# Kernel tuning notes

Measured on AMD Instinct MI355X. Metric: run time of the kernel, lower is better.

Reference implementation:

```python
import jax, jax.numpy as jnp
import numpy as np

B, T, C, H, N = 4, 2048, 1024, 16, 64
CHUNK = 256           # chunk_len
NBSWA = 2             # n_bswa_chunks
BSWA = CHUNK * NBSWA  # sliding window length
SSTATE = CHUNK        # kvm state slots (chunk_len * n_max_d_chunks)
SINK = 1              # sink_len
PARTIAL = 32          # rope_partial_dim
NEG = -1e30


def _ln(x, w, b, eps=1e-5):
    m = x.mean(-1, keepdims=True)
    v = jnp.mean((x - m) ** 2, -1, keepdims=True)
    return (x - m) * jax.lax.rsqrt(v + eps) * w + b


def _rope_tables():
    freq = (1.0 / 10000.0) ** np.linspace(0.0, 1.0, PARTIAL // 2, dtype=np.float32)
    freq = np.repeat(freq, 2)
    freq = np.concatenate([freq, np.zeros(N - PARTIAL, np.float32)])
    th = np.arange(T, dtype=np.float32)[:, None] * freq[None, :]
    cos = np.cos(th)
    sin = np.sin(th)
    sin[:, 1::2] *= -1.0
    return jnp.asarray(cos), jnp.asarray(sin)


def _rope(x, cos, sin):
    # pairwise flip (x0,x1)->(x1,x0)
    xf = x.reshape(*x.shape[:-1], N // 2, 2)[..., ::-1].reshape(x.shape)
    return cos[None, :, None, :] * x + sin[None, :, None, :] * xf


def _forward(residual, x, v1, x0, dx0,
             Wq, Wk, Wv, Wproj, Wkw,
             x_q, x_k, x_v, lamb,
             ln_q_w, ln_q_b, ln_k_w, ln_k_b, ln_dk_w, ln_dk_b, ln_res_w, ln_res_b,
             front_temp, state_temp):
    q = x @ Wq.T
    k = x @ Wk.T
    v = x @ Wv.T
    v = (1.0 - lamb) * v + lamb * v1  # value residual
    q = q.reshape(B, T, H, N)
    k = k.reshape(B, T, H, N)
    v = v.reshape(B, T, H, N)
    q = _ln(q, ln_q_w, ln_q_b)
    k = _ln(k, ln_k_w, ln_k_b)

    def shift(t):  # token shift (use_dkys=True variant)
        return jnp.concatenate([t[:, 0:1], t[:, :-1]], axis=1)

    q = q + x_q[None, None] * (shift(q) - q)
    k = k + x_k[None, None] * (shift(k) - k)
    v = v + x_v[None, None] * (shift(v) - v)

    cos, sin = _rope_tables()
    q = _rope(q, cos, sin)
    k = _rope(k, cos, sin)

    q = q.transpose(0, 2, 1, 3)  # [B,H,T,N]
    k = k.transpose(0, 2, 1, 3)
    v = v.transpose(0, 2, 1, 3)

    kw = jax.nn.sigmoid(jnp.einsum('btc,hc->bht', x, Wkw))[..., None]  # [B,H,T,1]
    st = state_temp.reshape(1, H, 1, 1)
    ft = front_temp.reshape(1, H, 1, 1)

    d_k = jnp.zeros((B, H, SSTATE, N), x.dtype)
    d_v = jnp.zeros((B, H, SSTATE, N), x.dtype)
    d_cnt = jnp.zeros((B, H, SSTATE, 1), x.dtype)
    scale = 1.0 / np.sqrt(N)
    outs = []
    for e in range(CHUNK, T + 1, CHUNK):  # fixed 8 chunks
        qb = e - CHUNK
        bb = max(0, e - BSWA)
        qc = q[:, :, qb:e]
        c_k = k[:, :, bb:bb + CHUNK]
        c_v = v[:, :, bb:bb + CHUNK]
        bk = k[:, :, bb:e]
        bv = v[:, :, bb:e]

        d_k_norm = _ln(d_k, ln_dk_w, ln_dk_b)
        d_vlen = d_cnt  # running count of accumulated c_v vectors per slot
        v_state = d_v / jnp.clip(jnp.linalg.norm(d_v, axis=-1, keepdims=True), 1e-12) * d_vlen
        k_star = jnp.concatenate([d_k_norm * st, bk * ft], axis=-2)
        v_star = jnp.concatenate([v_state, bv], axis=-2)

        qi = np.arange(qb, e)
        ki = np.arange(bb, e)
        mbias = np.where(ki[None, :] <= qi[:, None], 0.0, NEG).astype(np.float32)
        bias = jnp.asarray(np.concatenate([np.zeros((CHUNK, SSTATE), np.float32), mbias], axis=1))

        sc = jnp.einsum('bhqd,bhkd->bhqk', qc, k_star) * scale + bias
        out = jnp.einsum('bhqk,bhkd->bhqd', jax.nn.softmax(sc, axis=-1), v_star)
        outs.append(out)

        # state update: rope_zeroing on first PARTIAL channels, ln_d_k, nearest-slot scatter
        ck0 = jnp.concatenate([jnp.zeros_like(c_k[..., :PARTIAL]), c_k[..., PARTIAL:]], axis=-1)
        ck0 = _ln(ck0, ln_dk_w, ln_dk_b)
        sim = jnp.einsum('bhcd,bhsd->bhcs', ck0, d_k_norm)
        sim = sim.at[..., 0:SINK].set(NEG)
        kwc = kw[:, :, bb:bb + CHUNK]
        ck0 = ck0 * kwc
        cvw = c_v * kwc
        best = jnp.argmax(sim, axis=-1)                       # [B,H,CHUNK]
        oh = jax.nn.one_hot(best, SSTATE, dtype=x.dtype)      # [B,H,CHUNK,S]
        d_k = d_k + jnp.einsum('bhcs,bhcd->bhsd', oh, ck0)
        d_v = d_v + jnp.einsum('bhcs,bhcd->bhsd', oh, cvw)
        d_cnt = d_cnt + oh.sum(axis=2)[..., None]

    y = jnp.concatenate(outs, axis=2).transpose(0, 2, 1, 3).reshape(B, T, C)
    y = _ln(y, ln_res_w, ln_res_b)
    return residual + y @ Wproj.T


def setup_inputs() -> dict:
    key = jax.random.key(0)
    ks = jax.random.split(key, 12)
    f = lambda k, s, sc=1.0: jax.random.normal(k, s, dtype=jnp.float32) * sc
    return {
        'residual': f(ks[0], (B, T, C)),
        'x': f(ks[1], (B, T, C)),
        'v1': f(ks[2], (B, T, C)),
        'x0': f(ks[3], (B, T, C)),
        'dx0': f(ks[4], (B, T, C)),
        'token_ids': jax.random.randint(ks[5], (B, T), 0, 50257),
        'Wq': f(ks[6], (C, C), 0.02),
        'Wk': f(ks[7], (C, C), 0.02),
        'Wv': f(ks[8], (C, C), 0.02),
        'Wproj': f(ks[9], (C, C), 0.02),
        'Wkw': f(ks[10], (H, C), 0.02),
        'x_q': 0.5 * jnp.ones((H, N), jnp.float32),
        'x_k': 0.5 * jnp.ones((H, N), jnp.float32),
        'x_v': 0.5 * jnp.ones((H, N), jnp.float32),
        'lamb': jnp.float32(0.5),
        'ln_q_w': jnp.ones((N,), jnp.float32), 'ln_q_b': jnp.zeros((N,), jnp.float32),
        'ln_k_w': jnp.ones((N,), jnp.float32), 'ln_k_b': jnp.zeros((N,), jnp.float32),
        'ln_dk_w': jnp.ones((N,), jnp.float32), 'ln_dk_b': jnp.zeros((N,), jnp.float32),
        'ln_res_w': jnp.ones((C,), jnp.float32), 'ln_res_b': jnp.zeros((C,), jnp.float32),
        'front_temp': jnp.ones((H,), jnp.float32),
        'state_temp': jnp.ones((H,), jnp.float32),
    }


def reference(residual, x, v1, x0, dx0, token_ids,
              Wq, Wk, Wv, Wproj, Wkw, x_q, x_k, x_v, lamb,
              ln_q_w, ln_q_b, ln_k_w, ln_k_b, ln_dk_w, ln_dk_b, ln_res_w, ln_res_b,
              front_temp, state_temp):
    del token_ids  # unused in visible forward body
    return _forward(residual, x, v1, x0, dx0,
                    Wq, Wk, Wv, Wproj, Wkw,
                    x_q, x_k, x_v, lamb,
                    ln_q_w, ln_q_b, ln_k_w, ln_k_b, ln_dk_w, ln_dk_b, ln_res_w, ln_res_b,
                    front_temp, state_temp)
```

## Files before the change

### kernel.cpp

```cpp
#include <hip/hip_runtime.h>
#include <math.h>

#define Bq 4
#define Tq 2048
#define Cq 1024
#define Hq 16
#define Nq 64

typedef __attribute__((ext_vector_type(8))) short short8v;
typedef __attribute__((ext_vector_type(4))) float f32x4;

__device__ inline float waveSum(float v) {
#pragma unroll
  for (int o = 32; o; o >>= 1) v += __shfl_xor(v, o);
  return v;
}
__device__ inline unsigned short f2bf(float f) {
  unsigned u = __float_as_uint(f);
  unsigned r = (u + 0x7FFFu + ((u >> 16) & 1u)) >> 16;
  return (unsigned short)r;
}
__device__ inline float bf2f(unsigned short b) {
  return __uint_as_float(((unsigned)b) << 16);
}

__global__ __launch_bounds__(256) void f32_to_bf16_kernel(
    const float* __restrict__ src, unsigned short* __restrict__ dst, int n4)
{
  int i = blockIdx.x * 256 + threadIdx.x;
  if (i >= n4) return;
  float4 v = ((const float4*)src)[i];
  ushort4 o;
  o.x = f2bf(v.x); o.y = f2bf(v.y); o.z = f2bf(v.z); o.w = f2bf(v.w);
  ((ushort4*)dst)[i] = o;
}

__global__ __launch_bounds__(256) void f32_to_bf16_hilo_kernel(
    const float* __restrict__ src, unsigned short* __restrict__ hi,
    unsigned short* __restrict__ lo, int n4)
{
  int i = blockIdx.x * 256 + threadIdx.x;
  if (i >= n4) return;
  float4 v = ((const float4*)src)[i];
  ushort4 h, l;
  h.x = f2bf(v.x); l.x = f2bf(v.x - bf2f(h.x));
  h.y = f2bf(v.y); l.y = f2bf(v.y - bf2f(h.y));
  h.z = f2bf(v.z); l.z = f2bf(v.z - bf2f(h.z));
  h.w = f2bf(v.w); l.w = f2bf(v.w - bf2f(h.w));
  ((ushort4*)hi)[i] = h;
  ((ushort4*)lo)[i] = l;
}

__global__ __launch_bounds__(256) void gemm_bf16(
    const unsigned short* __restrict__ A, const unsigned short* __restrict__ W,
    float* __restrict__ dst, const float* __restrict__ extra,
    const float* __restrict__ lamb_p, int mode)
{
  const int m0 = blockIdx.x * 128, n0 = blockIdx.y * 128;
  const int tid = threadIdx.x;
  const int w = tid >> 6, l = tid & 63;
  const int wr = w >> 1, wc = w & 1;
  const int lrow = l & 15;
  const int lk = (l >> 4) * 8;

  f32x4 acc[4][4];
#pragma unroll
  for (int i = 0; i < 4; ++i)
#pragma unroll
    for (int j = 0; j < 4; ++j) acc[i][j] = (f32x4){0.f, 0.f, 0.f, 0.f};

  const unsigned short* Ab = A + (((size_t)(m0 + wr * 64 + lrow)) << 10) + lk;
  const unsigned short* Wb = W + (((size_t)(n0 + wc * 64 + lrow)) << 10) + lk;

  for (int k0 = 0; k0 < 1024; k0 += 32) {
    short8v a[4], b[4];
#pragma unroll
    for (int i = 0; i < 4; ++i) a[i] = *(const short8v*)(Ab + (((size_t)i) << 14) + k0);
#pragma unroll
    for (int j = 0; j < 4; ++j) b[j] = *(const short8v*)(Wb + (((size_t)j) << 14) + k0);
#pragma unroll
    for (int i = 0; i < 4; ++i)
#pragma unroll
      for (int j = 0; j < 4; ++j)
        acc[i][j] = __builtin_amdgcn_mfma_f32_16x16x32_bf16(a[i], b[j], acc[i][j], 0, 0, 0);
  }

  const float lam = (mode == 2) ? lamb_p[0] : 0.0f;
#pragma unroll
  for (int i = 0; i < 4; ++i)
#pragma unroll
    for (int j = 0; j < 4; ++j)
#pragma unroll
      for (int rg = 0; rg < 4; ++rg) {
        int m = m0 + wr * 64 + i * 16 + (l >> 4) * 4 + rg;
        int n = n0 + wc * 64 + j * 16 + (l & 15);
        float v = acc[i][j][rg];
        if (mode == 3) {
          dst[(size_t)m * Cq + n] = v + extra[(size_t)m * Cq + n];
        } else {
          if (mode == 2) v = (1.0f - lam) * v + lam * extra[(size_t)m * Cq + n];
          int b = m >> 11, t = m & (Tq - 1);
          int h = n >> 6, nn = n & 63;
          dst[((((size_t)b * Hq + h) * Tq + t) << 6) | nn] = v;
        }
      }
}

__global__ __launch_bounds__(256) void gemm_bf16_split(
    const unsigned short* __restrict__ Ah, const unsigned short* __restrict__ Al,
    const unsigned short* __restrict__ Wh, const unsigned short* __restrict__ Wl,
    float* __restrict__ dst)
{
  const int m0 = blockIdx.x * 128, n0 = blockIdx.y * 128;
  const int tid = threadIdx.x;
  const int w = tid >> 6, l = tid & 63;
  const int wr = w >> 1, wc = w & 1;
  const int lrow = l & 15;
  const int lk = (l >> 4) * 8;

  f32x4 acc[4][4];
#pragma unroll
  for (int i = 0; i < 4; ++i)
#pragma unroll
    for (int j = 0; j < 4; ++j) acc[i][j] = (f32x4){0.f, 0.f, 0.f, 0.f};

  const size_t aoff = (((size_t)(m0 + wr * 64 + lrow)) << 10) + lk;
  const size_t woff = (((size_t)(n0 + wc * 64 + lrow)) << 10) + lk;
  const unsigned short* Ahb = Ah + aoff;
  const unsigned short* Alb = Al + aoff;
  const unsigned short* Whb = Wh + woff;
  const unsigned short* Wlb = Wl + woff;

  for (int k0 = 0; k0 < 1024; k0 += 32) {
    short8v ah[4], al[4], bh[4], bl[4];
#pragma unroll
    for (int i = 0; i < 4; ++i) {
      ah[i] = *(const short8v*)(Ahb + (((size_t)i) << 14) + k0);
      al[i] = *(const short8v*)(Alb + (((size_t)i) << 14) + k0);
    }
#pragma unroll
    for (int j = 0; j < 4; ++j) {
      bh[j] = *(const short8v*)(Whb + (((size_t)j) << 14) + k0);
      bl[j] = *(const short8v*)(Wlb + (((size_t)j) << 14) + k0);
    }
#pragma unroll
    for (int i = 0; i < 4; ++i)
#pragma unroll
      for (int j = 0; j < 4; ++j) {
        acc[i][j] = __builtin_amdgcn_mfma_f32_16x16x32_bf16(ah[i], bh[j], acc[i][j], 0, 0, 0);
        acc[i][j] = __builtin_amdgcn_mfma_f32_16x16x32_bf16(ah[i], bl[j], acc[i][j], 0, 0, 0);
        acc[i][j] = __builtin_amdgcn_mfma_f32_16x16x32_bf16(al[i], bh[j], acc[i][j], 0, 0, 0);
      }
  }

#pragma unroll
  for (int i = 0; i < 4; ++i)
#pragma unroll
    for (int j = 0; j < 4; ++j)
#pragma unroll
      for (int rg = 0; rg < 4; ++rg) {
        int m = m0 + wr * 64 + i * 16 + (l >> 4) * 4 + rg;
        int n = n0 + wc * 64 + j * 16 + (l & 15);
        int b = m >> 11, t = m & (Tq - 1);
        int h = n >> 6, nn = n & 63;
        dst[((((size_t)b * Hq + h) * Tq + t) << 6) | nn] = acc[i][j][rg];
      }
}

__global__ __launch_bounds__(256) void postproc(
    const float* __restrict__ src, float* __restrict__ dst,
    unsigned short* __restrict__ dst_bf,
    const float* __restrict__ lnw, const float* __restrict__ lnb,
    const float* __restrict__ xs_p, int doLNRope)
{
  const int w = threadIdx.x >> 6, lane = threadIdx.x & 63;
  const int row = blockIdx.x * 4 + w;
  const int t = row & (Tq - 1);
  const int h = (row >> 11) & (Hq - 1);
  const size_t base = (size_t)row << 6;
  const size_t pbase = (t > 0) ? base - 64 : base;
  float cur = src[base + lane];
  float prv = src[pbase + lane];
  if (doLNRope) {
    const float lw = lnw[lane], lb = lnb[lane];
    {
      float m = waveSum(cur) * (1.0f / 64.0f);
      float d = cur - m;
      float var = waveSum(d * d) * (1.0f / 64.0f);
      cur = d * rsqrtf(var + 1e-5f) * lw + lb;
    }
    {
      float m = waveSum(prv) * (1.0f / 64.0f);
      float d = prv - m;
      float var = waveSum(d * d) * (1.0f / 64.0f);
      prv = d * rsqrtf(var + 1e-5f) * lw + lb;
    }
  }
  const float xv = xs_p[h * 64 + lane];
  float val = cur + xv * (prv - cur);
  if (doLNRope) {
    float partner = __shfl_xor(val, 1);
    if (lane < 32) {
      int i = lane >> 1;
      float freq = (float)exp((double)i * (-log(10000.0) / 15.0));
      float th = (float)t * freq;
      float c = cosf(th), s = sinf(th);
      val = c * val + ((lane & 1) ? -s : s) * partner;
    }
  }
  if (dst) dst[base + lane] = val;
  if (dst_bf) dst_bf[base + lane] = f2bf(val);
}

__global__ __launch_bounds__(256) void kw_kernel(
    const float* __restrict__ x, const float* __restrict__ Wkw, float* __restrict__ out)
{
  const int bt = blockIdx.x;
  const int tid = threadIdx.x, w = tid >> 6, lane = tid & 63;
  __shared__ float xs[Cq];
  for (int i = tid; i < Cq; i += 256) xs[i] = x[(size_t)bt * Cq + i];
  __syncthreads();
  const int b = bt >> 11, t = bt & (Tq - 1);
  for (int h = w; h < Hq; h += 4) {
    float acc = 0.0f;
    for (int i = lane; i < Cq; i += 64) acc += xs[i] * Wkw[h * Cq + i];
    acc = waveSum(acc);
    if (lane == 0) out[((size_t)(b * Hq + h)) * Tq + t] = 1.0f / (1.0f + expf(-acc));
  }
}

__global__ __launch_bounds__(1024, 1) void state_evolve_kernel(
    const float* __restrict__ kf, const unsigned short* __restrict__ v_bf,
    const float* __restrict__ kwp,
    unsigned short* __restrict__ dkn_bf, unsigned short* __restrict__ vst_bf,
    float* __restrict__ cnt_snap,
    const float* __restrict__ lnw, const float* __restrict__ lnb)
{
  const int bh = blockIdx.x;
  const int tid = threadIdx.x;
  const int s = tid >> 2, qd = tid & 3;
  const int db = qd * 16;
  const size_t seq = (size_t)Tq * Nq;
  const float* kb_ = kf + (size_t)bh * seq;
  const unsigned short* vb_ = v_bf + (size_t)bh * seq;
  const float* kwb = kwp + (size_t)bh * Tq;

  __shared__ float dknT[32 * 260];
  __shared__ float ck0T[32 * 260];
  __shared__ unsigned short VRow[256 * 72];
  __shared__ float Ps[256], Qs[256], aS[256], kwS[256];
  __shared__ float lwS[64], lbS[64];
  __shared__ int best[256];

  if (tid < 64) { lwS[tid] = lnw[tid]; lbS[tid] = lnb[tid]; }

  float dkReg[16], dvReg[16];
#pragma unroll
  for (int i = 0; i < 16; ++i) { dkReg[i] = 0.f; dvReg[i] = 0.f; }
  float cnt = 0.f;
  __syncthreads();

  for (int c = 0; c < 8; ++c) {
    const int e = c * 256 + 256;
    const int bb = (e - 512 > 0) ? (e - 512) : 0;

    {
      float sum = 0.f;
#pragma unroll
      for (int i = 0; i < 16; ++i) sum += dkReg[i];
      sum += __shfl_xor(sum, 1); sum += __shfl_xor(sum, 2);
      const float mean = sum * (1.0f / 64.0f);
      float sq = 0.f;
#pragma unroll
      for (int i = 0; i < 16; ++i) { float d = dkReg[i] - mean; sq += d * d; }
      sq += __shfl_xor(sq, 1); sq += __shfl_xor(sq, 2);
      const float rs = rsqrtf(sq * (1.0f / 64.0f) + 1e-5f);
      float kn[16];
#pragma unroll
      for (int i = 0; i < 16; ++i)
        kn[i] = (dkReg[i] - mean) * rs * lwS[db + i] + lbS[db + i];
      unsigned int pk[8];
#pragma unroll
      for (int i2 = 0; i2 < 8; ++i2)
        pk[i2] = (unsigned)f2bf(kn[2 * i2]) | ((unsigned)f2bf(kn[2 * i2 + 1]) << 16);
      unsigned short* kd = dkn_bf + (((size_t)bh * 8 + c) << 14) + s * 64 + db;
      *(uint4*)kd = make_uint4(pk[0], pk[1], pk[2], pk[3]);
      *(uint4*)(kd + 8) = make_uint4(pk[4], pk[5], pk[6], pk[7]);

      if (c > 0 && c < 7) {
        if (qd >= 2) {
#pragma unroll
          for (int i = 0; i < 16; ++i) dknT[(db - 32 + i) * 260 + s] = kn[i];
        } else {
          float pp = 0.f, qq = 0.f;
#pragma unroll
          for (int i = 0; i < 16; ++i) {
            pp += kn[i] * lwS[db + i];
            qq += kn[i] * lbS[db + i];
          }
          pp += __shfl_xor(pp, 1);
          qq += __shfl_xor(qq, 1);
          if (qd == 0) { Ps[s] = pp; Qs[s] = qq; }
        }
      }

      float sqv = 0.f;
#pragma unroll
      for (int i = 0; i < 16; ++i) sqv += dvReg[i] * dvReg[i];
      sqv += __shfl_xor(sqv, 1); sqv += __shfl_xor(sqv, 2);
      const float inrm = 1.0f / fmaxf(sqrtf(sqv), 1e-12f);
#pragma unroll
      for (int i2 = 0; i2 < 8; ++i2)
        pk[i2] = (unsigned)f2bf(dvReg[2 * i2] * inrm) |
                 ((unsigned)f2bf(dvReg[2 * i2 + 1] * inrm) << 16);
      unsigned short* vd = vst_bf + (((size_t)bh * 8 + c) << 14) + s * 64 + db;
      *(uint4*)vd = make_uint4(pk[0], pk[1], pk[2], pk[3]);
      *(uint4*)(vd + 8) = make_uint4(pk[4], pk[5], pk[6], pk[7]);
      if (qd == 0) cnt_snap[((size_t)bh * 8 + c) * 256 + s] = cnt;
    }

    if (c == 7) break;

    {
      float kv[16];
      if (qd >= 2) {
        const float* krow = kb_ + (size_t)(bb + s) * 64 + db;
#pragma unroll
        for (int i = 0; i < 16; i += 4) {
          float4 t4 = *(const float4*)(krow + i);
          kv[i] = t4.x; kv[i + 1] = t4.y; kv[i + 2] = t4.z; kv[i + 3] = t4.w;
        }
      } else {
#pragma unroll
        for (int i = 0; i < 16; ++i) kv[i] = 0.f;
      }
      float sum = 0.f;
#pragma unroll
      for (int i = 0; i < 16; ++i) sum += kv[i];
      sum += __shfl_xor(sum, 1); sum += __shfl_xor(sum, 2);
      const float mean = sum * (1.0f / 64.0f);
      float sq = 0.f;
#pragma unroll
      for (int i = 0; i < 16; ++i) { float d = kv[i] - mean; sq += d * d; }
      sq += __shfl_xor(sq, 1); sq += __shfl_xor(sq, 2);
      const float rs = rsqrtf(sq * (1.0f / 64.0f) + 1e-5f);
      if (qd >= 2) {
#pragma unroll
        for (int i = 0; i < 16; ++i)
          ck0T[(db - 32 + i) * 260 + s] =
              (kv[i] - mean) * rs * lwS[db + i] + lbS[db + i];
      }
      if (qd == 0) {
        aS[s] = (0.0f - mean) * rs;
        kwS[s] = kwb[bb + s];
      }
      const unsigned short* vsrc = vb_ + (size_t)(bb + s) * 64 + db;
      *(uint4*)&VRow[s * 72 + db] = *(const uint4*)vsrc;
      *(uint4*)&VRow[s * 72 + db + 8] = *(const uint4*)(vsrc + 8);
      if (c == 0 && tid < 256) best[tid] = 1;
    }
    __syncthreads();

    if (c > 0) {
      const int tx = tid & 31, ty = tid >> 5;
      const f32x4 pv0 = *(const f32x4*)&Ps[4 * tx];
      const f32x4 pv1 = *(const f32x4*)&Ps[128 + 4 * tx];
      const f32x4 qv0 = *(const f32x4*)&Qs[4 * tx];
      const f32x4 qv1 = *(const f32x4*)&Qs[128 + 4 * tx];
#pragma unroll
      for (int pass = 0; pass < 2; ++pass) {
        const int rc0 = pass * 128 + ty * 4;
        float a4[4];
#pragma unroll
        for (int i = 0; i < 4; ++i) a4[i] = aS[rc0 + i];
        float acc[4][8];
#pragma unroll
        for (int i = 0; i < 4; ++i)
#pragma unroll
          for (int j = 0; j < 4; ++j) {
            acc[i][j] = a4[i] * pv0[j] + qv0[j];
            acc[i][j + 4] = a4[i] * pv1[j] + qv1[j];
          }
#pragma unroll 4
        for (int k = 0; k < 32; ++k) {
          f32x4 av = *(const f32x4*)&ck0T[k * 260 + rc0];
          f32x4 b0 = *(const f32x4*)&dknT[k * 260 + 4 * tx];
          f32x4 b1 = *(const f32x4*)&dknT[k * 260 + 128 + 4 * tx];
#pragma unroll
          for (int i = 0; i < 4; ++i)
#pragma unroll
            for (int j = 0; j < 4; ++j) {
              acc[i][j] += av[i] * b0[j];
              acc[i][j + 4] += av[i] * b1[j];
            }
        }
#pragma unroll
        for (int i = 0; i < 4; ++i) {
          float bvv = -3.0e38f;
          int bi = 1 << 30;
#pragma unroll
          for (int j = 0; j < 8; ++j) {
            int s2 = (j < 4) ? (4 * tx + j) : (128 + 4 * tx + (j - 4));
            float v = acc[i][j];
            if (s2 == 0) v = -1.0e30f;
            if (v > bvv || (v == bvv && s2 < bi)) { bvv = v; bi = s2; }
          }
#pragma unroll
          for (int o = 16; o; o >>= 1) {
            float ov = __shfl_xor(bvv, o);
            int oi = __shfl_xor(bi, o);
            if (ov > bvv || (ov == bvv && oi < bi)) { bvv = ov; bi = oi; }
          }
          if (tx == 0) best[rc0 + i] = bi;
        }
      }
      __syncthreads();
    }

    {
      int cadd = 0;
      for (int rc = 0; rc < 256; ++rc) {
        if (best[rc] == s) {
          const float kwv = kwS[rc];
          if (qd < 2) {
            const float a = aS[rc];
#pragma unroll
            for (int i = 0; i < 16; ++i)
              dkReg[i] += (a * lwS[db + i] + lbS[db + i]) * kwv;
          } else {
#pragma unroll
            for (int i = 0; i < 16; ++i)
              dkReg[i] += ck0T[(db - 32 + i) * 260 + rc] * kwv;
          }
          const uint4 u0 = *(const uint4*)&VRow[rc * 72 + db];
          const uint4 u1 = *(const uint4*)&VRow[rc * 72 + db + 8];
          const unsigned uu[8] = {u0.x, u0.y, u0.z, u0.w, u1.x, u1.y, u1.z, u1.w};
#pragma unroll
          for (int i2 = 0; i2 < 8; ++i2) {
            dvReg[2 * i2] += __uint_as_float((uu[i2] & 0xFFFFu) << 16) * kwv;
            dvReg[2 * i2 + 1] += __uint_as_float(uu[i2] & 0xFFFF0000u) * kwv;
          }
          ++cadd;
        }
      }
      cnt += (float)cadd;
    }
    __syncthreads();
  }
}

__global__ __launch_bounds__(256, 2) void attn_mfma_kernel(
    const unsigned short* __restrict__ q_bf, const unsigned short* __restrict__ k_bf,
    const unsigned short* __restrict__ v_bf,
    const unsigned short* __restrict__ dkn_bf, const unsigned short* __restrict__ vst_bf,
    const float* __restrict__ cnt_snap, float* __restrict__ y,
    const float* __restrict__ ftp, const float* __restrict__ stp)
{
  const int blk = blockIdx.x;
  const int bh = blk >> 4;
  const int c = (blk >> 1) & 7;
  const int half = blk & 1;
  const int h = bh & (Hq - 1);
  const int tid = threadIdx.x;
  const int w = tid >> 6, l = tid & 63;
  const int g = l >> 4, n = l & 15;
  const int rows0 = c * 256 + half * 128 + w * 32;
  const int e = c * 256 + 256;
  const int bb = (e - 512 > 0) ? (e - 512) : 0;
  const int nwt = (e - bb) >> 6;
  const float stsc = stp[h] * 0.125f, ftsc = ftp[h] * 0.125f;
  const size_t seq = (size_t)Tq * Nq;

  __shared__ unsigned short Ks[64 * 72];
  __shared__ unsigned short VTs[64 * 72];
  __shared__ unsigned short Ps[4][32 * 72];
  __shared__ float wts[64];

  short8v qf[2][2];
#pragma unroll
  for (int mt = 0; mt < 2; ++mt)
#pragma unroll
    for (int kh = 0; kh < 2; ++kh)
      qf[mt][kh] = *(const short8v*)(q_bf + (size_t)bh * seq +
                                     (size_t)(rows0 + mt * 16 + n) * 64 + kh * 32 + g * 8);

  f32x4 oacc[2][4];
#pragma unroll
  for (int mt = 0; mt < 2; ++mt)
#pragma unroll
    for (int dt = 0; dt < 4; ++dt) oacc[mt][dt] = (f32x4){0.f, 0.f, 0.f, 0.f};
  float rowM[2][4], rowL[2][4];
#pragma unroll
  for (int mt = 0; mt < 2; ++mt)
#pragma unroll
    for (int r = 0; r < 4; ++r) { rowM[mt][r] = -1.0e30f; rowL[mt][r] = 0.f; }

  const int nkt = 4 + nwt;
  for (int kt = 0; kt < nkt; ++kt) {
    const bool isState = kt < 4;
    const int t0 = isState ? kt * 64 : bb + (kt - 4) * 64;
    const unsigned short* ksrc = isState
        ? dkn_bf + (((size_t)bh * 8 + c) << 14) + (size_t)t0 * 64
        : k_bf + (size_t)bh * seq + (size_t)t0 * 64;
    const unsigned short* vsrc = isState
        ? vst_bf + (((size_t)bh * 8 + c) << 14) + (size_t)t0 * 64
        : v_bf + (size_t)bh * seq + (size_t)t0 * 64;

    __syncthreads();
    {
      const int row = tid >> 2, q4 = tid & 3;
      const unsigned short* src = ksrc + row * 64 + q4 * 16;
      *(uint4*)&Ks[row * 72 + q4 * 16] = *(const uint4*)src;
      *(uint4*)&Ks[row * 72 + q4 * 16 + 8] = *(const uint4*)(src + 8);
      const unsigned short* vs = vsrc + row * 64 + q4 * 16;
#pragma unroll
      for (int i = 0; i < 16; ++i) VTs[(q4 * 16 + i) * 72 + row] = vs[i];
      if (tid < 64)
        wts[tid] = isState ? cnt_snap[((size_t)bh * 8 + c) * 256 + kt * 64 + tid] : 1.0f;
    }
    __syncthreads();

    f32x4 sacc[2][4];
#pragma unroll
    for (int mt = 0; mt < 2; ++mt)
#pragma unroll
      for (int nt = 0; nt < 4; ++nt) sacc[mt][nt] = (f32x4){0.f, 0.f, 0.f, 0.f};
#pragma unroll
    for (int nt = 0; nt < 4; ++nt) {
      short8v kf0 = *(const short8v*)&Ks[(nt * 16 + n) * 72 + g * 8];
      short8v kf1 = *(const short8v*)&Ks[(nt * 16 + n) * 72 + 32 + g * 8];
#pragma unroll
      for (int mt = 0; mt < 2; ++mt) {
        sacc[mt][nt] = __builtin_amdgcn_mfma_f32_16x16x32_bf16(qf[mt][0], kf0, sacc[mt][nt], 0, 0, 0);
        sacc[mt][nt] = __builtin_amdgcn_mfma_f32_16x16x32_bf16(qf[mt][1], kf1, sacc[mt][nt], 0, 0, 0);
      }
    }

    const float scale = isState ? stsc : ftsc;
    float wt_n[4];
#pragma unroll
    for (int nt = 0; nt < 4; ++nt) wt_n[nt] = wts[nt * 16 + n];

#pragma unroll
    for (int mt = 0; mt < 2; ++mt) {
#pragma unroll
      for (int r = 0; r < 4; ++r) {
        float sv[4];
#pragma unroll
        for (int nt = 0; nt < 4; ++nt) {
          float s = sacc[mt][nt][r] * scale;
          if (!isState) {
            int qi = rows0 + mt * 16 + g * 4 + r;
            int kj = t0 + nt * 16 + n;
            if (kj > qi) s = -1.0e30f;
          }
          sv[nt] = s;
        }
        float tmax = fmaxf(fmaxf(sv[0], sv[1]), fmaxf(sv[2], sv[3]));
        tmax = fmaxf(tmax, __shfl_xor(tmax, 1));
        tmax = fmaxf(tmax, __shfl_xor(tmax, 2));
        tmax = fmaxf(tmax, __shfl_xor(tmax, 4));
        tmax = fmaxf(tmax, __shfl_xor(tmax, 8));
        const float Mold = rowM[mt][r];
        const float Mnew = fmaxf(Mold, tmax);
        const float al = __expf(Mold - Mnew);
        rowM[mt][r] = Mnew;
        float p[4], ts = 0.f;
#pragma unroll
        for (int nt = 0; nt < 4; ++nt) { p[nt] = __expf(sv[nt] - Mnew); ts += p[nt]; }
        ts += __shfl_xor(ts, 1);
        ts += __shfl_xor(ts, 2);
        ts += __shfl_xor(ts, 4);
        ts += __shfl_xor(ts, 8);
        rowL[mt][r] = rowL[mt][r] * al + ts;
#pragma unroll
        for (int dt = 0; dt < 4; ++dt) oacc[mt][dt][r] *= al;
        const int prow = (mt * 16 + g * 4 + r) * 72;
#pragma unroll
        for (int nt = 0; nt < 4; ++nt)
          Ps[w][prow + nt * 16 + n] = f2bf(p[nt] * wt_n[nt]);
      }
    }

    short8v pf[2][2];
#pragma unroll
    for (int mt = 0; mt < 2; ++mt)
#pragma unroll
      for (int jh = 0; jh < 2; ++jh)
        pf[mt][jh] = *(const short8v*)&Ps[w][(mt * 16 + n) * 72 + jh * 32 + g * 8];
#pragma unroll
    for (int dt = 0; dt < 4; ++dt) {
      short8v vf0 = *(const short8v*)&VTs[(dt * 16 + n) * 72 + g * 8];
      short8v vf1 = *(const short8v*)&VTs[(dt * 16 + n) * 72 + 32 + g * 8];
#pragma unroll
      for (int mt = 0; mt < 2; ++mt) {
        oacc[mt][dt] = __builtin_amdgcn_mfma_f32_16x16x32_bf16(pf[mt][0], vf0, oacc[mt][dt], 0, 0, 0);
        oacc[mt][dt] = __builtin_amdgcn_mfma_f32_16x16x32_bf16(pf[mt][1], vf1, oacc[mt][dt], 0, 0, 0);
      }
    }
  }

#pragma unroll
  for (int mt = 0; mt < 2; ++mt) {
#pragma unroll
    for (int r = 0; r < 4; ++r) {
      const float inv = 1.0f / rowL[mt][r];
      const int row = rows0 + mt * 16 + g * 4 + r;
#pragma unroll
      for (int dt = 0; dt < 4; ++dt)
        y[(size_t)bh * seq + (size_t)row * 64 + dt * 16 + n] = oacc[mt][dt][r] * inv;
    }
  }
}

__global__ __launch_bounds__(256) void final_ln(
    const float* __restrict__ y, const float* __restrict__ lnw,
    const float* __restrict__ lnb, unsigned short* __restrict__ dst)
{
  const int bt = blockIdx.x;
  const int b = bt >> 11, t = bt & (Tq - 1);
  const int tid = threadIdx.x, w = tid >> 6, lane = tid & 63;
  __shared__ float red[8];
  float v[4];
  float s = 0.0f;
#pragma unroll
  for (int i = 0; i < 4; ++i) {
    int c = tid + (i << 8);
    int h = c >> 6, n = c & 63;
    v[i] = y[((((size_t)b * Hq + h) * Tq + t) << 6) + n];
    s += v[i];
  }
  s = waveSum(s);
  if (lane == 0) red[w] = s;
  __syncthreads();
  const float mean = (red[0] + red[1] + red[2] + red[3]) * (1.0f / 1024.0f);
  float s2 = 0.0f;
#pragma unroll
  for (int i = 0; i < 4; ++i) { float d = v[i] - mean; s2 += d * d; }
  s2 = waveSum(s2);
  if (lane == 0) red[4 + w] = s2;
  __syncthreads();
  const float var = (red[4] + red[5] + red[6] + red[7]) * (1.0f / 1024.0f);
  const float rs = rsqrtf(var + 1e-5f);
#pragma unroll
  for (int i = 0; i < 4; ++i) {
    int c = tid + (i << 8);
    dst[(size_t)bt * Cq + c] = f2bf((v[i] - mean) * rs * lnw[c] + lnb[c]);
  }
}

extern "C" void kernel_launch(void* const* d_in, const int* in_sizes, int n_in,
                              void* d_out, int out_size, void* d_ws, size_t ws_size,
                              hipStream_t stream)
{
  (void)in_sizes; (void)n_in; (void)out_size; (void)ws_size;
  const float* residual = (const float*)d_in[0];
  const float* x        = (const float*)d_in[1];
  const float* v1       = (const float*)d_in[2];
  const float* Wq       = (const float*)d_in[6];
  const float* Wk       = (const float*)d_in[7];
  const float* Wv       = (const float*)d_in[8];
  const float* Wproj    = (const float*)d_in[9];
  const float* Wkw      = (const float*)d_in[10];
  const float* x_q      = (const float*)d_in[11];
  const float* x_k      = (const float*)d_in[12];
  const float* x_v      = (const float*)d_in[13];
  const float* lamb     = (const float*)d_in[14];
  const float* ln_q_w   = (const float*)d_in[15];
  const float* ln_q_b   = (const float*)d_in[16];
  const float* ln_k_w   = (const float*)d_in[17];
  const float* ln_k_b   = (const float*)d_in[18];
  const float* ln_dk_w  = (const float*)d_in[19];
  const float* ln_dk_b  = (const float*)d_in[20];
  const float* ln_res_w = (const float*)d_in[21];
  const float* ln_res_b = (const float*)d_in[22];
  const float* ftp      = (const float*)d_in[23];
  const float* stp      = (const float*)d_in[24];

  float* ws = (float*)d_ws;
  const size_t SZ = (size_t)Bq * Hq * Tq * Nq;
  float* q_raw = ws;
  float* ybuf  = ws;
  float* k_raw = ws + SZ;
  unsigned short* vst_bf = (unsigned short*)(ws + SZ);
  float* cnt_snap = ws + SZ + SZ / 2;
  float* v_mix = ws + 2 * SZ;
  unsigned short* ylnb_bf = (unsigned short*)(ws + 2 * SZ);
  float* k_fin = ws + 3 * SZ;
  unsigned short* q_bf = (unsigned short*)(ws + 4 * SZ);
  unsigned short* x_lo = q_bf;
  unsigned short* k_bf = q_bf + SZ;
  unsigned short* wk_hi = k_bf;
  unsigned short* wk_lo = wk_hi + (1u << 20);
  unsigned short* v_bf = (unsigned short*)(ws + 5 * SZ);
  unsigned short* xb   = v_bf + SZ;
  unsigned short* dkn_bf = xb;
  unsigned short* wqb = (unsigned short*)(ws + 6 * SZ);
  unsigned short* wvb = wqb + (1u << 20);
  unsigned short* wpb = wvb + (1u << 20);
  float* kwbuf = ws + 6 * SZ + ((3u << 20) >> 1);

  dim3 gb(256);
  dim3 ggb(64, 8);

  hipLaunchKernelGGL(f32_to_bf16_hilo_kernel, dim3((int)(SZ / 4 / 256)), gb, 0, stream,
                     x, xb, x_lo, (int)(SZ / 4));
  hipLaunchKernelGGL(f32_to_bf16_hilo_kernel, dim3(1024), gb, 0, stream,
                     Wk, wk_hi, wk_lo, 262144);
  hipLaunchKernelGGL(f32_to_bf16_kernel, dim3(1024), gb, 0, stream, Wq, wqb, 262144);
  hipLaunchKernelGGL(f32_to_bf16_kernel, dim3(1024), gb, 0, stream, Wv, wvb, 262144);
  hipLaunchKernelGGL(f32_to_bf16_kernel, dim3(1024), gb, 0, stream, Wproj, wpb, 262144);

  hipLaunchKernelGGL(gemm_bf16, ggb, gb, 0, stream, xb, wqb, q_raw, (const float*)nullptr, lamb, 1);
  hipLaunchKernelGGL(gemm_bf16_split, ggb, gb, 0, stream, xb, x_lo, wk_hi, wk_lo, k_raw);
  hipLaunchKernelGGL(gemm_bf16, ggb, gb, 0, stream, xb, wvb, v_mix, v1, lamb, 2);
  hipLaunchKernelGGL(kw_kernel, dim3(Bq * Tq), gb, 0, stream, x, Wkw, kwbuf);

  const int rows = Bq * Hq * Tq;
  hipLaunchKernelGGL(postproc, dim3(rows / 4), gb, 0, stream, q_raw, (float*)nullptr, q_bf, ln_q_w, ln_q_b, x_q, 1);
  hipLaunchKernelGGL(postproc, dim3(rows / 4), gb, 0, stream, k_raw, k_fin, k_bf, ln_k_w, ln_k_b, x_k, 1);
  hipLaunchKernelGGL(postproc, dim3(rows / 4), gb, 0, stream, v_mix, (float*)nullptr, v_bf,
                     (const float*)nullptr, (const float*)nullptr, x_v, 0);

  hipLaunchKernelGGL(state_evolve_kernel, dim3(Bq * Hq), dim3(1024), 0, stream,
                     k_fin, v_bf, kwbuf, dkn_bf, vst_bf, cnt_snap, ln_dk_w, ln_dk_b);

  hipLaunchKernelGGL(attn_mfma_kernel, dim3(Bq * Hq * 16), gb, 0, stream,
                     q_bf, k_bf, v_bf, dkn_bf, vst_bf, cnt_snap, ybuf, ftp, stp);

  hipLaunchKernelGGL(final_ln, dim3(Bq * Tq), gb, 0, stream, ybuf, ln_res_w, ln_res_b, ylnb_bf);
  hipLaunchKernelGGL(gemm_bf16, ggb, gb, 0, stream, ylnb_bf, wpb, (float*)d_out, residual, lamb, 3);
}
```

Measured before the change: 1.405 ms.

## Use split-bf16 MFMA for state argmax similarity and count-guided scatter

New measurement: 1.983 ms. 1.41x slower.

```diff
diff --git a/kernel.cpp b/kernel.cpp
--- a/kernel.cpp
+++ b/kernel.cpp
@@ -245,12 +245,16 @@
   const unsigned short* vb_ = v_bf + (size_t)bh * seq;
   const float* kwb = kwp + (size_t)bh * Tq;
 
-  __shared__ float dknT[32 * 260];
-  __shared__ float ck0T[32 * 260];
-  __shared__ unsigned short VRow[256 * 72];
-  __shared__ float Ps[256], Qs[256], aS[256], kwS[256];
+  __shared__ unsigned short ck0h[256 * 72];
+  __shared__ unsigned short ck0l[256 * 72];
+  __shared__ unsigned short dknh[256 * 72];
+  __shared__ unsigned short dknl[256 * 72];
   __shared__ float lwS[64], lbS[64];
+  __shared__ float kwS[256];
   __shared__ int best[256];
+  __shared__ int cntS[256];
+  __shared__ float candV[4][256];
+  __shared__ int candI[4][256];
 
   if (tid < 64) { lwS[tid] = lnw[tid]; lbS[tid] = lnb[tid]; }
 
@@ -279,29 +283,28 @@
 #pragma unroll
       for (int i = 0; i < 16; ++i)
         kn[i] = (dkReg[i] - mean) * rs * lwS[db + i] + lbS[db + i];
-      unsigned int pk[8];
+      unsigned short h16[16], l16[16];
+#pragma unroll
+      for (int i = 0; i < 16; ++i) {
+        h16[i] = f2bf(kn[i]);
+        l16[i] = f2bf(kn[i] - bf2f(h16[i]));
+      }
+      unsigned pk[8];
 #pragma unroll
       for (int i2 = 0; i2 < 8; ++i2)
-        pk[i2] = (unsigned)f2bf(kn[2 * i2]) | ((unsigned)f2bf(kn[2 * i2 + 1]) << 16);
+        pk[i2] = (unsigned)h16[2 * i2] | ((unsigned)h16[2 * i2 + 1] << 16);
       unsigned short* kd = dkn_bf + (((size_t)bh * 8 + c) << 14) + s * 64 + db;
       *(uint4*)kd = make_uint4(pk[0], pk[1], pk[2], pk[3]);
       *(uint4*)(kd + 8) = make_uint4(pk[4], pk[5], pk[6], pk[7]);
-
-      if (c > 0 && c < 7) {
-        if (qd >= 2) {
-#pragma unroll
-          for (int i = 0; i < 16; ++i) dknT[(db - 32 + i) * 260 + s] = kn[i];
-        } else {
-          float pp = 0.f, qq = 0.f;
-#pragma unroll
-          for (int i = 0; i < 16; ++i) {
-            pp += kn[i] * lwS[db + i];
-            qq += kn[i] * lbS[db + i];
-          }
-          pp += __shfl_xor(pp, 1);
-          qq += __shfl_xor(qq, 1);
-          if (qd == 0) { Ps[s] = pp; Qs[s] = qq; }
-        }
+      if (c >= 1 && c <= 6) {
+        *(uint4*)&dknh[s * 72 + db] = make_uint4(pk[0], pk[1], pk[2], pk[3]);
+        *(uint4*)&dknh[s * 72 + db + 8] = make_uint4(pk[4], pk[5], pk[6], pk[7]);
+        unsigned pl[8];
+#pragma unroll
+        for (int i2 = 0; i2 < 8; ++i2)
+          pl[i2] = (unsigned)l16[2 * i2] | ((unsigned)l16[2 * i2 + 1] << 16);
+        *(uint4*)&dknl[s * 72 + db] = make_uint4(pl[0], pl[1], pl[2], pl[3]);
+        *(uint4*)&dknl[s * 72 + db + 8] = make_uint4(pl[4], pl[5], pl[6], pl[7]);
       }
 
       float sqv = 0.f;
@@ -309,13 +312,14 @@
       for (int i = 0; i < 16; ++i) sqv += dvReg[i] * dvReg[i];
       sqv += __shfl_xor(sqv, 1); sqv += __shfl_xor(sqv, 2);
       const float inrm = 1.0f / fmaxf(sqrtf(sqv), 1e-12f);
+      unsigned pv[8];
 #pragma unroll
       for (int i2 = 0; i2 < 8; ++i2)
-        pk[i2] = (unsigned)f2bf(dvReg[2 * i2] * inrm) |
+        pv[i2] = (unsigned)f2bf(dvReg[2 * i2] * inrm) |
                  ((unsigned)f2bf(dvReg[2 * i2 + 1] * inrm) << 16);
       unsigned short* vd = vst_bf + (((size_t)bh * 8 + c) << 14) + s * 64 + db;
-      *(uint4*)vd = make_uint4(pk[0], pk[1], pk[2], pk[3]);
-      *(uint4*)(vd + 8) = make_uint4(pk[4], pk[5], pk[6], pk[7]);
+      *(uint4*)vd = make_uint4(pv[0], pv[1], pv[2], pv[3]);
+      *(uint4*)(vd + 8) = make_uint4(pv[4], pv[5], pv[6], pv[7]);
       if (qd == 0) cnt_snap[((size_t)bh * 8 + c) * 256 + s] = cnt;
     }
 
@@ -344,106 +348,136 @@
       for (int i = 0; i < 16; ++i) { float d = kv[i] - mean; sq += d * d; }
       sq += __shfl_xor(sq, 1); sq += __shfl_xor(sq, 2);
       const float rs = rsqrtf(sq * (1.0f / 64.0f) + 1e-5f);
-      if (qd >= 2) {
-#pragma unroll
-        for (int i = 0; i < 16; ++i)
-          ck0T[(db - 32 + i) * 260 + s] =
-              (kv[i] - mean) * rs * lwS[db + i] + lbS[db + i];
-      }
-      if (qd == 0) {
-        aS[s] = (0.0f - mean) * rs;
-        kwS[s] = kwb[bb + s];
-      }
-      const unsigned short* vsrc = vb_ + (size_t)(bb + s) * 64 + db;
-      *(uint4*)&VRow[s * 72 + db] = *(const uint4*)vsrc;
-      *(uint4*)&VRow[s * 72 + db + 8] = *(const uint4*)(vsrc + 8);
-      if (c == 0 && tid < 256) best[tid] = 1;
+      unsigned short h16[16], l16[16];
+#pragma unroll
+      for (int i = 0; i < 16; ++i) {
+        float cv = (kv[i] - mean) * rs * lwS[db + i] + lbS[db + i];
+        h16[i] = f2bf(cv);
+        l16[i] = f2bf(cv - bf2f(h16[i]));
+      }
+      unsigned ph[8], pl[8];
+#pragma unroll
+      for (int i2 = 0; i2 < 8; ++i2) {
+        ph[i2] = (unsigned)h16[2 * i2] | ((unsigned)h16[2 * i2 + 1] << 16);
+        pl[i2] = (unsigned)l16[2 * i2] | ((unsigned)l16[2 * i2 + 1] << 16);
+      }
+      *(uint4*)&ck0h[s * 72 + db] = make_uint4(ph[0], ph[1], ph[2], ph[3]);
+      *(uint4*)&ck0h[s * 72 + db + 8] = make_uint4(ph[4], ph[5], ph[6], ph[7]);
+      *(uint4*)&ck0l[s * 72 + db] = make_uint4(pl[0], pl[1], pl[2], pl[3]);
+      *(uint4*)&ck0l[s * 72 + db + 8] = make_uint4(pl[4], pl[5], pl[6], pl[7]);
+      if (qd == 0) kwS[s] = kwb[bb + s];
+      if (tid < 256) {
+        if (c == 0) { best[tid] = 1; cntS[tid] = (tid == 1) ? 256 : 0; }
+        else cntS[tid] = 0;
+      }
     }
     __syncthreads();
 
     if (c > 0) {
-      const int tx = tid & 31, ty = tid >> 5;
-      const f32x4 pv0 = *(const f32x4*)&Ps[4 * tx];
-      const f32x4 pv1 = *(const f32x4*)&Ps[128 + 4 * tx];
-      const f32x4 qv0 = *(const f32x4*)&Qs[4 * tx];
-      const f32x4 qv1 = *(const f32x4*)&Qs[128 + 4 * tx];
-#pragma unroll
-      for (int pass = 0; pass < 2; ++pass) {
-        const int rc0 = pass * 128 + ty * 4;
-        float a4[4];
-#pragma unroll
-        for (int i = 0; i < 4; ++i) a4[i] = aS[rc0 + i];
-        float acc[4][8];
-#pragma unroll
-        for (int i = 0; i < 4; ++i)
+      const int w = tid >> 6, l = tid & 63;
+      const int Rb = (w & 3) * 64, Sb = (w >> 2) * 64;
+      const int lrow = l & 15, lko = (l >> 4) * 8;
+#pragma unroll
+      for (int p = 0; p < 4; ++p) {
+        const int arow = (Rb + p * 16 + lrow) * 72 + lko;
+        const short8v ah0 = *(const short8v*)&ck0h[arow];
+        const short8v ah1 = *(const short8v*)&ck0h[arow + 32];
+        const short8v al0 = *(const short8v*)&ck0l[arow];
+        const short8v al1 = *(const short8v*)&ck0l[arow + 32];
+        f32x4 sacc[4];
+#pragma unroll
+        for (int j = 0; j < 4; ++j) sacc[j] = (f32x4){0.f, 0.f, 0.f, 0.f};
+#pragma unroll
+        for (int j = 0; j < 4; ++j) {
+          const int brow = (Sb + j * 16 + lrow) * 72 + lko;
+          const short8v bh0 = *(const short8v*)&dknh[brow];
+          const short8v bh1 = *(const short8v*)&dknh[brow + 32];
+          const short8v bl0 = *(const short8v*)&dknl[brow];
+          const short8v bl1 = *(const short8v*)&dknl[brow + 32];
+          sacc[j] = __builtin_amdgcn_mfma_f32_16x16x32_bf16(ah0, bh0, sacc[j], 0, 0, 0);
+          sacc[j] = __builtin_amdgcn_mfma_f32_16x16x32_bf16(ah1, bh1, sacc[j], 0, 0, 0);
+          sacc[j] = __builtin_amdgcn_mfma_f32_16x16x32_bf16(ah0, bl0, sacc[j], 0, 0, 0);
+          sacc[j] = __builtin_amdgcn_mfma_f32_16x16x32_bf16(ah1, bl1, sacc[j], 0, 0, 0);
+          sacc[j] = __builtin_amdgcn_mfma_f32_16x16x32_bf16(al0, bh0, sacc[j], 0, 0, 0);
+          sacc[j] = __builtin_amdgcn_mfma_f32_16x16x32_bf16(al1, bh1, sacc[j], 0, 0, 0);
+        }
+#pragma unroll
+        for (int r = 0; r < 4; ++r) {
+          float bv = -3.0e38f;
+          int bi = 1 << 30;
 #pragma unroll
           for (int j = 0; j < 4; ++j) {
-            acc[i][j] = a4[i] * pv0[j] + qv0[j];
-            acc[i][j + 4] = a4[i] * pv1[j] + qv1[j];
+            const int s2 = Sb + j * 16 + lrow;
+            float v = sacc[j][r];
+            if (s2 == 0) v = -1.0e30f;
+            if (v > bv || (v == bv && s2 < bi)) { bv = v; bi = s2; }
           }
-#pragma unroll 4
-        for (int k = 0; k < 32; ++k) {
-          f32x4 av = *(const f32x4*)&ck0T[k * 260 + rc0];
-          f32x4 b0 = *(const f32x4*)&dknT[k * 260 + 4 * tx];
-          f32x4 b1 = *(const f32x4*)&dknT[k * 260 + 128 + 4 * tx];
-#pragma unroll
-          for (int i = 0; i < 4; ++i)
-#pragma unroll
-            for (int j = 0; j < 4; ++j) {
-              acc[i][j] += av[i] * b0[j];
-              acc[i][j + 4] += av[i] * b1[j];
+#pragma unroll
+          for (int o = 1; o <= 8; o <<= 1) {
+            float ov = __shfl_xor(bv, o);
+            int oi = __shfl_xor(bi, o);
+            if (ov > bv || (ov == bv && oi < bi)) { bv = ov; bi = oi; }
+          }
+          if (lrow == 0) {
+            const int rc = Rb + p * 16 + (l >> 4) * 4 + r;
+            candV[w >> 2][rc] = bv;
+            candI[w >> 2][rc] = bi;
+          }
+        }
+      }
+      __syncthreads();
+      if (tid < 256) {
+        float bv = candV[0][tid];
+        int bi = candI[0][tid];
+#pragma unroll
+        for (int g = 1; g < 4; ++g) {
+          float v = candV[g][tid];
+          int i2 = candI[g][tid];
+          if (v > bv || (v == bv && i2 < bi)) { bv = v; bi = i2; }
+        }
+        best[tid] = bi;
+        atomicAdd(&cntS[bi], 1);
+      }
+      __syncthreads();
+    }
+
+    {
+      const int need = cntS[s];
+      if (need) {
+        int found = 0;
+        for (int rc = 0; rc < 256 && found < need; ++rc) {
+          if (best[rc] == s) {
+            const float kwv = kwS[rc];
+            const int cb = rc * 72 + db;
+            const uint4 h0 = *(const uint4*)&ck0h[cb];
+            const uint4 h1 = *(const uint4*)&ck0h[cb + 8];
+            const uint4 l0 = *(const uint4*)&ck0l[cb];
+            const uint4 l1 = *(const uint4*)&ck0l[cb + 8];
+            const unsigned hh[8] = {h0.x, h0.y, h0.z, h0.w, h1.x, h1.y, h1.z, h1.w};
+            const unsigned ll[8] = {l0.x, l0.y, l0.z, l0.w, l1.x, l1.y, l1.z, l1.w};
+#pragma unroll
+            for (int i2 = 0; i2 < 8; ++i2) {
+              float c0 = __uint_as_float((hh[i2] & 0xFFFFu) << 16) +
+                         __uint_as_float((ll[i2] & 0xFFFFu) << 16);
+              float c1 = __uint_as_float(hh[i2] & 0xFFFF0000u) +
+                         __uint_as_float(ll[i2] & 0xFFFF0000u);
+              dkReg[2 * i2] += c0 * kwv;
+              dkReg[2 * i2 + 1] += c1 * kwv;
             }
+            const unsigned short* vr = vb_ + (size_t)(bb + rc) * 64 + db;
+            const uint4 v0 = *(const uint4*)vr;
+            const uint4 v1 = *(const uint4*)(vr + 8);
+            const unsigned vv[8] = {v0.x, v0.y, v0.z, v0.w, v1.x, v1.y, v1.z, v1.w};
+#pragma unroll
+            for (int i2 = 0; i2 < 8; ++i2) {
+              dvReg[2 * i2] += __uint_as_float((vv[i2] & 0xFFFFu) << 16) * kwv;
+              dvReg[2 * i2 + 1] += __uint_as_float(vv[i2] & 0xFFFF0000u) * kwv;
+            }
+            ++found;
+          }
         }
-#pragma unroll
-        for (int i = 0; i < 4; ++i) {
-          float bvv = -3.0e38f;
-          int bi = 1 << 30;
-#pragma unroll
-          for (int j = 0; j < 8; ++j) {
-            int s2 = (j < 4) ? (4 * tx + j) : (128 + 4 * tx + (j - 4));
-            float v = acc[i][j];
-            if (s2 == 0) v = -1.0e30f;
-            if (v > bvv || (v == bvv && s2 < bi)) { bvv = v; bi = s2; }
-          }
-#pragma unroll
-          for (int o = 16; o; o >>= 1) {
-            float ov = __shfl_xor(bvv, o);
-            int oi = __shfl_xor(bi, o);
-            if (ov > bvv || (ov == bvv && oi < bi)) { bvv = ov; bi = oi; }
-          }
-          if (tx == 0) best[rc0 + i] = bi;
-        }
-      }
-      __syncthreads();
-    }
-
-    {
-      int cadd = 0;
-      for (int rc = 0; rc < 256; ++rc) {
-        if (best[rc] == s) {
-          const float kwv = kwS[rc];
-          if (qd < 2) {
-            const float a = aS[rc];
-#pragma unroll
-            for (int i = 0; i < 16; ++i)
-              dkReg[i] += (a * lwS[db + i] + lbS[db + i]) * kwv;
-          } else {
-#pragma unroll
-            for (int i = 0; i < 16; ++i)
-              dkReg[i] += ck0T[(db - 32 + i) * 260 + rc] * kwv;
-          }
-          const uint4 u0 = *(const uint4*)&VRow[rc * 72 + db];
-          const uint4 u1 = *(const uint4*)&VRow[rc * 72 + db + 8];
-          const unsigned uu[8] = {u0.x, u0.y, u0.z, u0.w, u1.x, u1.y, u1.z, u1.w};
-#pragma unroll
-          for (int i2 = 0; i2 < 8; ++i2) {
-            dvReg[2 * i2] += __uint_as_float((uu[i2] & 0xFFFFu) << 16) * kwv;
-            dvReg[2 * i2 + 1] += __uint_as_float(uu[i2] & 0xFFFF0000u) * kwv;
-          }
-          ++cadd;
-        }
-      }
-      cnt += (float)cadd;
+        cnt += (float)need;
+      }
     }
     __syncthreads();
   }
```

## Double-buffer GEMM operand loads and skip empty slots in state scatter

Applied to the files above, without the earlier changes.

Result: slower. 1.510 ms (+7.5%).

```diff
diff --git a/kernel.cpp b/kernel.cpp
--- a/kernel.cpp
+++ b/kernel.cpp
@@ -72,17 +72,34 @@
   const unsigned short* Ab = A + (((size_t)(m0 + wr * 64 + lrow)) << 10) + lk;
   const unsigned short* Wb = W + (((size_t)(n0 + wc * 64 + lrow)) << 10) + lk;
 
-  for (int k0 = 0; k0 < 1024; k0 += 32) {
-    short8v a[4], b[4];
-#pragma unroll
-    for (int i = 0; i < 4; ++i) a[i] = *(const short8v*)(Ab + (((size_t)i) << 14) + k0);
-#pragma unroll
-    for (int j = 0; j < 4; ++j) b[j] = *(const short8v*)(Wb + (((size_t)j) << 14) + k0);
+  short8v aA[4], bA[4], aB[4], bB[4];
+#pragma unroll
+  for (int i = 0; i < 4; ++i) aA[i] = *(const short8v*)(Ab + (((size_t)i) << 14));
+#pragma unroll
+  for (int j = 0; j < 4; ++j) bA[j] = *(const short8v*)(Wb + (((size_t)j) << 14));
+
+#pragma unroll
+  for (int k0 = 0; k0 < 1024; k0 += 64) {
+#pragma unroll
+    for (int i = 0; i < 4; ++i) aB[i] = *(const short8v*)(Ab + (((size_t)i) << 14) + k0 + 32);
+#pragma unroll
+    for (int j = 0; j < 4; ++j) bB[j] = *(const short8v*)(Wb + (((size_t)j) << 14) + k0 + 32);
 #pragma unroll
     for (int i = 0; i < 4; ++i)
 #pragma unroll
       for (int j = 0; j < 4; ++j)
-        acc[i][j] = __builtin_amdgcn_mfma_f32_16x16x32_bf16(a[i], b[j], acc[i][j], 0, 0, 0);
+        acc[i][j] = __builtin_amdgcn_mfma_f32_16x16x32_bf16(aA[i], bA[j], acc[i][j], 0, 0, 0);
+    if (k0 + 64 < 1024) {
+#pragma unroll
+      for (int i = 0; i < 4; ++i) aA[i] = *(const short8v*)(Ab + (((size_t)i) << 14) + k0 + 64);
+#pragma unroll
+      for (int j = 0; j < 4; ++j) bA[j] = *(const short8v*)(Wb + (((size_t)j) << 14) + k0 + 64);
+    }
+#pragma unroll
+    for (int i = 0; i < 4; ++i)
+#pragma unroll
+      for (int j = 0; j < 4; ++j)
+        acc[i][j] = __builtin_amdgcn_mfma_f32_16x16x32_bf16(aB[i], bB[j], acc[i][j], 0, 0, 0);
   }
 
   const float lam = (mode == 2) ? lamb_p[0] : 0.0f;
@@ -131,25 +148,49 @@
   const unsigned short* Whb = Wh + woff;
   const unsigned short* Wlb = Wl + woff;
 
-  for (int k0 = 0; k0 < 1024; k0 += 32) {
-    short8v ah[4], al[4], bh[4], bl[4];
+  short8v ahA[4], alA[4], bhA[4], blA[4];
+  short8v ahB[4], alB[4], bhB[4], blB[4];
+#pragma unroll
+  for (int i = 0; i < 4; ++i) {
+    ahA[i] = *(const short8v*)(Ahb + (((size_t)i) << 14));
+    alA[i] = *(const short8v*)(Alb + (((size_t)i) << 14));
+    bhA[i] = *(const short8v*)(Whb + (((size_t)i) << 14));
+    blA[i] = *(const short8v*)(Wlb + (((size_t)i) << 14));
+  }
+
+#pragma unroll
+  for (int k0 = 0; k0 < 1024; k0 += 64) {
 #pragma unroll
     for (int i = 0; i < 4; ++i) {
-      ah[i] = *(const short8v*)(Ahb + (((size_t)i) << 14) + k0);
-      al[i] = *(const short8v*)(Alb + (((size_t)i) << 14) + k0);
-    }
-#pragma unroll
-    for (int j = 0; j < 4; ++j) {
-      bh[j] = *(const short8v*)(Whb + (((size_t)j) << 14) + k0);
-      bl[j] = *(const short8v*)(Wlb + (((size_t)j) << 14) + k0);
+      ahB[i] = *(const short8v*)(Ahb + (((size_t)i) << 14) + k0 + 32);
+      alB[i] = *(const short8v*)(Alb + (((size_t)i) << 14) + k0 + 32);
+      bhB[i] = *(const short8v*)(Whb + (((size_t)i) << 14) + k0 + 32);
+      blB[i] = *(const short8v*)(Wlb + (((size_t)i) << 14) + k0 + 32);
     }
 #pragma unroll
     for (int i = 0; i < 4; ++i)
 #pragma unroll
       for (int j = 0; j < 4; ++j) {
-        acc[i][j] = __builtin_amdgcn_mfma_f32_16x16x32_bf16(ah[i], bh[j], acc[i][j], 0, 0, 0);
-        acc[i][j] = __builtin_amdgcn_mfma_f32_16x16x32_bf16(ah[i], bl[j], acc[i][j], 0, 0, 0);
-        acc[i][j] = __builtin_amdgcn_mfma_f32_16x16x32_bf16(al[i], bh[j], acc[i][j], 0, 0, 0);
+        acc[i][j] = __builtin_amdgcn_mfma_f32_16x16x32_bf16(ahA[i], bhA[j], acc[i][j], 0, 0, 0);
+        acc[i][j] = __builtin_amdgcn_mfma_f32_16x16x32_bf16(ahA[i], blA[j], acc[i][j], 0, 0, 0);
+        acc[i][j] = __builtin_amdgcn_mfma_f32_16x16x32_bf16(alA[i], bhA[j], acc[i][j], 0, 0, 0);
+      }
+    if (k0 + 64 < 1024) {
+#pragma unroll
+      for (int i = 0; i < 4; ++i) {
+        ahA[i] = *(const short8v*)(Ahb + (((size_t)i) << 14) + k0 + 64);
+        alA[i] = *(const short8v*)(Alb + (((size_t)i) << 14) + k0 + 64);
+        bhA[i] = *(const short8v*)(Whb + (((size_t)i) << 14) + k0 + 64);
+        blA[i] = *(const short8v*)(Wlb + (((size_t)i) << 14) + k0 + 64);
+      }
+    }
+#pragma unroll
+    for (int i = 0; i < 4; ++i)
+#pragma unroll
+      for (int j = 0; j < 4; ++j) {
+        acc[i][j] = __builtin_amdgcn_mfma_f32_16x16x32_bf16(ahB[i], bhB[j], acc[i][j], 0, 0, 0);
+        acc[i][j] = __builtin_amdgcn_mfma_f32_16x16x32_bf16(ahB[i], blB[j], acc[i][j], 0, 0, 0);
+        acc[i][j] = __builtin_amdgcn_mfma_f32_16x16x32_bf16(alB[i], bhB[j], acc[i][j], 0, 0, 0);
       }
   }
 
@@ -251,6 +292,7 @@
   __shared__ float Ps[256], Qs[256], aS[256], kwS[256];
   __shared__ float lwS[64], lbS[64];
   __shared__ int best[256];
+  __shared__ int cntS[256];
 
   if (tid < 64) { lwS[tid] = lnw[tid]; lbS[tid] = lnb[tid]; }
 
@@ -357,7 +399,10 @@
       const unsigned short* vsrc = vb_ + (size_t)(bb + s) * 64 + db;
       *(uint4*)&VRow[s * 72 + db] = *(const uint4*)vsrc;
       *(uint4*)&VRow[s * 72 + db + 8] = *(const uint4*)(vsrc + 8);
-      if (c == 0 && tid < 256) best[tid] = 1;
+      if (tid < 256) {
+        if (c == 0) { best[tid] = 1; cntS[tid] = (tid == 1) ? 256 : 0; }
+        else cntS[tid] = 0;
+      }
     }
     __syncthreads();
 
@@ -411,39 +456,45 @@
             int oi = __shfl_xor(bi, o);
             if (ov > bvv || (ov == bvv && oi < bi)) { bvv = ov; bi = oi; }
           }
-          if (tx == 0) best[rc0 + i] = bi;
+          if (tx == 0) {
+            best[rc0 + i] = bi;
+            atomicAdd(&cntS[bi], 1);
+          }
         }
       }
       __syncthreads();
     }
 
     {
-      int cadd = 0;
-      for (int rc = 0; rc < 256; ++rc) {
-        if (best[rc] == s) {
-          const float kwv = kwS[rc];
-          if (qd < 2) {
-            const float a = aS[rc];
-#pragma unroll
-            for (int i = 0; i < 16; ++i)
-              dkReg[i] += (a * lwS[db + i] + lbS[db + i]) * kwv;
-          } else {
-#pragma unroll
-            for (int i = 0; i < 16; ++i)
-              dkReg[i] += ck0T[(db - 32 + i) * 260 + rc] * kwv;
+      const int need = cntS[s];
+      if (need) {
+        int found = 0;
+        for (int rc = 0; rc < 256 && found < need; ++rc) {
+          if (best[rc] == s) {
+            const float kwv = kwS[rc];
+            if (qd < 2) {
+              const float a = aS[rc];
+#pragma unroll
+              for (int i = 0; i < 16; ++i)
+                dkReg[i] += (a * lwS[db + i] + lbS[db + i]) * kwv;
+            } else {
+#pragma unroll
+              for (int i = 0; i < 16; ++i)
+                dkReg[i] += ck0T[(db - 32 + i) * 260 + rc] * kwv;
+            }
+            const uint4 u0 = *(const uint4*)&VRow[rc * 72 + db];
+            const uint4 u1 = *(const uint4*)&VRow[rc * 72 + db + 8];
+            const unsigned uu[8] = {u0.x, u0.y, u0.z, u0.w, u1.x, u1.y, u1.z, u1.w};
+#pragma unroll
+            for (int i2 = 0; i2 < 8; ++i2) {
+              dvReg[2 * i2] += __uint_as_float((uu[i2] & 0xFFFFu) << 16) * kwv;
+              dvReg[2 * i2 + 1] += __uint_as_float(uu[i2] & 0xFFFF0000u) * kwv;
+            }
+            ++found;
           }
-          const uint4 u0 = *(const uint4*)&VRow[rc * 72 + db];
-          const uint4 u1 = *(const uint4*)&VRow[rc * 72 + db + 8];
-          const unsigned uu[8] = {u0.x, u0.y, u0.z, u0.w, u1.x, u1.y, u1.z, u1.w};
-#pragma unroll
-          for (int i2 = 0; i2 < 8; ++i2) {
-            dvReg[2 * i2] += __uint_as_float((uu[i2] & 0xFFFFu) << 16) * kwv;
-            dvReg[2 * i2 + 1] += __uint_as_float(uu[i2] & 0xFFFF0000u) * kwv;
-          }
-          ++cadd;
         }
-      }
-      cnt += (float)cadd;
+        cnt += (float)need;
+      }
     }
     __syncthreads();
   }
```
